# Optimization experiments

Hardware: AMD Instinct MI355X
Metric: run time of the kernel (lower is better)

The kernel has to match this reference:

```python
import jax, jax.numpy as jnp
import numpy as np

D = 768
CTX = 64


def ln(x, g, b, eps=1e-5):
    m = x.mean(-1, keepdims=True)
    v = jnp.mean((x - m) ** 2, -1, keepdims=True)
    return (x - m) / jnp.sqrt(v + eps) * g + b


def setup_inputs() -> dict:
    key = jax.random.key(0)
    ks = jax.random.split(key, 16)
    B, N = 16, 1024
    w = lambda k, shape: jax.random.normal(k, shape, dtype=jnp.float32) * 0.02
    return {
        'comps': jax.random.normal(ks[0], (8, B, N, D), jnp.float32),
        'geometric_context': jax.random.normal(ks[1], (B, N, D), jnp.float32),
        'question_features': jax.random.normal(ks[2], (B, D), jnp.float32),
        'spatial_mask': jax.random.randint(ks[3], (B,), 0, 2) > 0,
        'gp_w1': w(ks[4], (D, D // 2)), 'gp_b1': jnp.zeros((D // 2,)),
        'gp_g1': jnp.ones((D // 2,)), 'gp_be1': jnp.zeros((D // 2,)),
        'gp_w2': w(ks[5], (D // 2, CTX)), 'gp_b2': jnp.zeros((CTX,)),
        'swp_w1': w(ks[6], (CTX + D, 256)), 'swp_b1': jnp.zeros((256,)),
        'swp_g1': jnp.ones((256,)), 'swp_be1': jnp.zeros((256,)),
        'swp_w2': w(ks[7], (256, 128)), 'swp_b2': jnp.zeros((128,)),
        'swp_g2': jnp.ones((128,)), 'swp_be2': jnp.zeros((128,)),
        'swp_w3': w(ks[8], (128, 8)), 'swp_b3': jnp.zeros((8,)),
        'sw1': w(ks[9], (4, D + CTX, D)), 'sb1': jnp.zeros((4, D)),
        'sg1': jnp.ones((4, D)), 'sbe1': jnp.zeros((4, D)),
        'sw2': w(ks[10], (4, D, D)), 'sb2': jnp.zeros((4, D)),
        'sg2': jnp.ones((4, D)), 'sbe2': jnp.zeros((4, D)),
        'rw1': w(ks[11], (4, D + CTX, D)), 'rb1': jnp.zeros((4, D)),
        'rg1': jnp.ones((4, D)), 'rbe1': jnp.zeros((4, D)),
        'rw2': w(ks[12], (4, D, D)), 'rb2': jnp.zeros((4, D)),
    }


def reference(comps, geometric_context, question_features, spatial_mask,
              gp_w1, gp_b1, gp_g1, gp_be1, gp_w2, gp_b2,
              swp_w1, swp_b1, swp_g1, swp_be1, swp_w2, swp_b2, swp_g2, swp_be2, swp_w3, swp_b3,
              sw1, sb1, sg1, sbe1, sw2, sb2, sg2, sbe2,
              rw1, rb1, rg1, rbe1, rw2, rb2):
    B, N = geometric_context.shape[:2]
    # geometric_processor on mean-pooled context -> [B, 64]
    gcc = jax.nn.relu(ln(geometric_context.mean(1) @ gp_w1 + gp_b1, gp_g1, gp_be1)) @ gp_w2 + gp_b2
    # spatial_weight_predictor -> softmax weights [B, 8]
    wi = jnp.concatenate([gcc, question_features], -1)
    h = jax.nn.gelu(ln(wi @ swp_w1 + swp_b1, swp_g1, swp_be1), approximate=False)
    h = jax.nn.gelu(ln(h @ swp_w2 + swp_b2, swp_g2, swp_be2), approximate=False)
    aw = jax.nn.softmax(h @ swp_w3 + swp_b3, -1)
    # expanded context; non-spatial samples use 0.1-scaled context for spatial-set comps
    ctx = jnp.broadcast_to(gcc[:, None, :], (B, N, CTX))
    ctx_s = ctx * jnp.where(spatial_mask, 1.0, 0.1)[:, None, None]
    # strong enhancers (GELU, second LN): P_unique(0), V_unique(1), PV(3), PT(5) - all spatial-set
    xs = jnp.concatenate([comps[jnp.array([0, 1, 3, 5])],
                          jnp.broadcast_to(ctx_s, (4, B, N, CTX))], -1)
    h = jax.nn.gelu(ln(jnp.einsum('kbnd,kdf->kbnf', xs, sw1) + sb1[:, None, None, :],
                       sg1[:, None, None, :], sbe1[:, None, None, :]), approximate=False)
    ys = ln(jnp.einsum('kbnd,kdf->kbnf', h, sw2) + sb2[:, None, None, :],
            sg2[:, None, None, :], sbe2[:, None, None, :])
    # ReLU enhancers (moderate/minimal share structure): TV(4, scaled ctx), T_unique(2), redundant(6), higher(7)
    ctx_r = jnp.stack([ctx_s, ctx, ctx, ctx], 0)
    xr = jnp.concatenate([comps[jnp.array([4, 2, 6, 7])], ctx_r], -1)
    h = jax.nn.relu(ln(jnp.einsum('kbnd,kdf->kbnf', xr, rw1) + rb1[:, None, None, :],
                       rg1[:, None, None, :], rbe1[:, None, None, :]))
    yr = jnp.einsum('kbnd,kdf->kbnf', h, rw2) + rb2[:, None, None, :]
    # non-spatial components pass through when spatial_mask is False
    m = spatial_mask[:, None, None]
    out = jnp.stack([
        ys[0],                              # P_unique
        ys[1],                              # V_unique
        jnp.where(m, yr[1], comps[2]),      # T_unique
        ys[2],                              # PV_synergy
        yr[0],                              # TV_synergy
        ys[3],                              # PT_synergy
        jnp.where(m, yr[2], comps[6]),      # redundant
        jnp.where(m, yr[3], comps[7]),      # higher_synergy
    ], 0)
    return out, aw
```

## Files before the change

### kernel.cpp

```cpp
#include <hip/hip_runtime.h>
#include <math.h>

#define MT 16384
#define DD 768
#define AW_OFF ((size_t)8 * MT * DD)

typedef __attribute__((ext_vector_type(8))) short short8;
typedef __attribute__((ext_vector_type(4))) float f32x4;
typedef __attribute__((ext_vector_type(4))) float fv4;
typedef __attribute__((ext_vector_type(4))) unsigned int u32x4;

#define OFF_W1T 0ULL
#define OFF_W2T 9437184ULL
#define OFF_Z1  19660800ULL
#define OFF_Z2  220987392ULL
#define OFF_P1  321650688ULL
#define OFF_P2  327942144ULL
#define OFF_ST1 331087872ULL
#define OFF_ST2 332136448ULL
#define OFF_GP  332660736ULL
#define OFF_GM  333053952ULL
#define OFF_CXF 333103104ULL
#define OFF_B1X 333111296ULL
#define OFF_A1  335544320ULL
#define OFF_CB  536870912ULL

static __device__ __forceinline__ unsigned short f2bf(float f) {
  unsigned u = __float_as_uint(f);
  u += 0x7fffu + ((u >> 16) & 1u);
  return (unsigned short)(u >> 16);
}
static __device__ __forceinline__ float bf2f(unsigned short h) {
  return __uint_as_float(((unsigned)h) << 16);
}
static __device__ __forceinline__ unsigned pk2(float lo, float hi) {
  return (unsigned)f2bf(lo) | ((unsigned)f2bf(hi) << 16);
}
static __device__ __forceinline__ float gelu_t(float y) {
  float y2 = y * y;
  float c = fmaf(y2, 0.0713548163f, 1.59576912161f);
  float e = __expf(-y * c);
  return y / (1.0f + e);
}
static __device__ __forceinline__ void gload_lds16(const void* g, void* l) {
  __builtin_amdgcn_global_load_lds(
      (const __attribute__((address_space(1))) void*)g,
      (__attribute__((address_space(3))) void*)l, 16, 0, 0);
}

__global__ void cvt_comps(const float* __restrict__ c,
                          unsigned short* __restrict__ cb, long n8) {
  long i = (long)blockIdx.x * blockDim.x + threadIdx.x;
  const long stride = (long)gridDim.x * blockDim.x;
  for (; i < n8; i += stride) {
    const fv4* p = (const fv4*)(c + i * 8);
    fv4 a = p[0], b = p[1];
    u32x4 v;
    v[0] = pk2(a[0], a[1]); v[1] = pk2(a[2], a[3]);
    v[2] = pk2(b[0], b[1]); v[3] = pk2(b[2], b[3]);
    *(u32x4*)(cb + i * 8) = v;
  }
}

__global__ void transpose_cvt(const float* sw1, const float* rw1,
                              const float* sw2, const float* rw2,
                              unsigned short* w1T, unsigned short* w2T) {
  __shared__ float t[32][33];
  const int z = blockIdx.z;
  const float* sp; unsigned short* dp;
  if (z < 8) {
    sp = ((z < 4) ? sw1 : rw1) + (size_t)(z & 3) * 832 * DD;
    dp = w1T + (size_t)z * DD * DD;
  } else {
    int zz = z - 8;
    sp = ((zz < 4) ? sw2 : rw2) + (size_t)(zz & 3) * DD * DD;
    dp = w2T + (size_t)zz * DD * DD;
  }
  const int r0 = blockIdx.x * 32, c0 = blockIdx.y * 32;
  const int tx = threadIdx.x & 31, ty = threadIdx.x >> 5;
#pragma unroll
  for (int i = 0; i < 4; i++) {
    int r = ty + i * 8;
    t[r][tx] = sp[(size_t)(r0 + r) * DD + c0 + tx];
  }
  __syncthreads();
#pragma unroll
  for (int i = 0; i < 4; i++) {
    int cc = ty + i * 8;
    dp[(size_t)(c0 + cc) * DD + r0 + tx] = f2bf(t[tx][cc]);
  }
}

__global__ void colmean1(const float* __restrict__ geo, float* __restrict__ gp) {
  const int b = blockIdx.z, yc = blockIdx.y;
  const int col = blockIdx.x * 256 + threadIdx.x;
  const float* p = geo + (size_t)b * 1024 * DD + (size_t)yc * 128 * DD + col;
  float s = 0.f;
  for (int n = 0; n < 128; ++n) s += p[(size_t)n * DD];
  gp[((size_t)b * 8 + yc) * DD + col] = s;
}
__global__ void colmean2(const float* __restrict__ gp, float* __restrict__ gm) {
  const int b = blockIdx.y;
  const int col = blockIdx.x * 256 + threadIdx.x;
  float s = 0.f;
#pragma unroll
  for (int i = 0; i < 8; ++i) s += gp[((size_t)b * 8 + i) * DD + col];
  gm[(size_t)b * DD + col] = s * (1.0f / 1024.0f);
}

static __device__ float2 blk_sum2(float a, float b, float* red) {
  const int tid = threadIdx.x;
  __syncthreads();
  red[tid] = a; red[512 + tid] = b;
  if (tid < 128) { red[384 + tid] = 0.f; red[512 + 384 + tid] = 0.f; }
  __syncthreads();
  for (int s = 256; s > 0; s >>= 1) {
    if (tid < s) { red[tid] += red[tid + s]; red[512 + tid] += red[512 + tid + s]; }
    __syncthreads();
  }
  return make_float2(red[0], red[512]);
}

__global__ void small_mlp(
    const float* __restrict__ gc_mean, const float* __restrict__ qf,
    const int* __restrict__ mask,
    const float* __restrict__ gp_w1, const float* __restrict__ gp_b1,
    const float* __restrict__ gp_g1, const float* __restrict__ gp_be1,
    const float* __restrict__ gp_w2, const float* __restrict__ gp_b2,
    const float* __restrict__ swp_w1, const float* __restrict__ swp_b1,
    const float* __restrict__ swp_g1, const float* __restrict__ swp_be1,
    const float* __restrict__ swp_w2, const float* __restrict__ swp_b2,
    const float* __restrict__ swp_g2, const float* __restrict__ swp_be2,
    const float* __restrict__ swp_w3, const float* __restrict__ swp_b3,
    float* __restrict__ cxfs, float* __restrict__ cxfu,
    float* __restrict__ aw)
{
  __shared__ float gm[768];
  __shared__ float buf[832];
  __shared__ float tmp[384];
  __shared__ float red[1024];
  const int b = blockIdx.x, tid = threadIdx.x;

  for (int i = tid; i < 768; i += 384) gm[i] = gc_mean[b * 768 + i];
  __syncthreads();

  float z = gp_b1[tid];
  for (int k = 0; k < 768; k++) z += gm[k] * gp_w1[k * 384 + tid];
  float2 s = blk_sum2(z, z * z, red);
  {
    float mean = s.x * (1.f / 384.f);
    float rinv = rsqrtf(s.y * (1.f / 384.f) - mean * mean + 1e-5f);
    float y = (z - mean) * rinv * gp_g1[tid] + gp_be1[tid];
    tmp[tid] = fmaxf(y, 0.f);
  }
  __syncthreads();

  if (tid < 64) {
    float g = gp_b2[tid];
    for (int k = 0; k < 384; k++) g += tmp[k] * gp_w2[k * 64 + tid];
    float sc = (mask[b] != 0) ? 1.0f : 0.1f;
    cxfs[b * 64 + tid] = g * sc;
    cxfu[b * 64 + tid] = g;
    buf[tid] = g;
  }
  for (int i = tid; i < 768; i += 384) buf[64 + i] = qf[b * 768 + i];
  __syncthreads();

  float z1 = 0.f;
  if (tid < 256) {
    z1 = swp_b1[tid];
    for (int k = 0; k < 832; k++) z1 += buf[k] * swp_w1[k * 256 + tid];
  }
  s = blk_sum2(z1, z1 * z1, red);
  {
    float mean = s.x * (1.f / 256.f);
    float rinv = rsqrtf(s.y * (1.f / 256.f) - mean * mean + 1e-5f);
    if (tid < 256) {
      float y = (z1 - mean) * rinv * swp_g1[tid] + swp_be1[tid];
      tmp[tid] = 0.5f * y * (1.f + erff(y * 0.7071067811865476f));
    }
  }
  __syncthreads();

  float z2 = 0.f;
  if (tid < 128) {
    z2 = swp_b2[tid];
    for (int k = 0; k < 256; k++) z2 += tmp[k] * swp_w2[k * 128 + tid];
  }
  s = blk_sum2(z2, z2 * z2, red);
  {
    float mean = s.x * (1.f / 128.f);
    float rinv = rsqrtf(s.y * (1.f / 128.f) - mean * mean + 1e-5f);
    if (tid < 128) {
      float y = (z2 - mean) * rinv * swp_g2[tid] + swp_be2[tid];
      tmp[tid] = 0.5f * y * (1.f + erff(y * 0.7071067811865476f));
    }
  }
  __syncthreads();

  if (tid < 8) {
    float z3 = swp_b3[tid];
    for (int k = 0; k < 128; k++) z3 += tmp[k] * swp_w3[k * 8 + tid];
    buf[tid] = z3;
  }
  __syncthreads();
  if (tid < 8) {
    float mx = buf[0];
    for (int k = 1; k < 8; k++) mx = fmaxf(mx, buf[k]);
    float ssum = 0.f;
    for (int k = 0; k < 8; k++) ssum += expf(buf[k] - mx);
    aw[b * 8 + tid] = expf(buf[tid] - mx) / ssum;
  }
}

__global__ void ctxbias_k(const float* __restrict__ cxfs,
                          const float* __restrict__ cxfu,
                          const float* __restrict__ sw1, const float* __restrict__ rw1,
                          const float* __restrict__ sb1, const float* __restrict__ rb1,
                          float* __restrict__ b1x)
{
  const int br = blockIdx.x, b = blockIdx.y, tid = threadIdx.x;
  __shared__ float cf[64];
  if (tid < 64) cf[tid] = ((br <= 4) ? cxfs : cxfu)[b * 64 + tid];
  __syncthreads();
  const float* W = ((br < 4) ? sw1 + (size_t)br * 832 * DD
                             : rw1 + (size_t)(br - 4) * 832 * DD) + (size_t)768 * DD;
  const float* bb = (br < 4) ? sb1 + br * DD : rb1 + (br - 4) * DD;
#pragma unroll
  for (int jj = 0; jj < 3; ++jj) {
    const int f = tid + jj * 256;
    float s = bb[f];
    for (int k = 0; k < 64; ++k) s += cf[k] * W[(size_t)k * DD + f];
    b1x[((size_t)br * 16 + b) * DD + f] = s;
  }
}

__global__ void stats_k(const float2* __restrict__ part, float2* __restrict__ st,
                        int nr) {
  int i = blockIdx.x * 256 + threadIdx.x;
  if (i >= nr) return;
  float s1 = 0.f, s2 = 0.f;
#pragma unroll
  for (int s = 0; s < 3; ++s) {
    float2 p = part[(size_t)s * nr + i];
    s1 += p.x; s2 += p.y;
  }
  float mean = s1 * (1.f / 768.f);
  float var = s2 * (1.f / 768.f) - mean * mean;
  float rinv = rsqrtf(var + 1e-5f);
  st[i] = make_float2(rinv, -mean * rinv);
}

__global__ __launch_bounds__(512, 4)
void gemm1_k(const unsigned short* __restrict__ compsb,
             const unsigned short* __restrict__ w1T,
             const float* __restrict__ b1x,
             unsigned short* __restrict__ z1,
             float2* __restrict__ part1,
             const int* __restrict__ mask)
{
  __shared__ __align__(16) unsigned short As[3][4096];
  __shared__ __align__(16) unsigned short Bs[3][8192];
  __shared__ float pscr[4][128][2];
  constexpr int NT = 24;

  const int id = blockIdx.x;
  const int x = id & 7, j = id >> 3;
  const int br_nt = j >> 4;
  const int mt = ((j & 15) << 3) | x;
  const int nt = br_nt % 3;
  const int br = br_nt / 3;
  const int m0 = mt * 128, n0 = nt * 256;
  const int b = m0 >> 10;
  if (br >= 5 && mask[b] == 0) return;

  const int ci = (0x76245310u >> (br * 4)) & 15;
  const unsigned short* az = compsb + (size_t)ci * MT * DD + (size_t)m0 * DD;
  const unsigned short* wT = w1T + (size_t)br * DD * DD + (size_t)n0 * DD;

  const int tid = threadIdx.x;
  const int w = tid >> 6, lane = tid & 63, llo = lane & 15, lhi = lane >> 4;
  const int wm = w & 1, wn = w >> 1;
  const int q = lane & 3, rrB = w * 16 + (lane >> 2);
  const int swqB = q ^ ((rrB >> 1) & 3);

  const unsigned short* asrcD = az + (size_t)rrB * DD + swqB * 8;
  const unsigned short* bsrc0 = wT + (size_t)rrB * DD + swqB * 8;
  const unsigned short* bsrc1 = wT + (size_t)(128 + rrB) * DD + swqB * 8;

  f32x4 acc[4][4];
#pragma unroll
  for (int mf = 0; mf < 4; ++mf)
#pragma unroll
    for (int nf = 0; nf < 4; ++nf) acc[mf][nf] = (f32x4)0.0f;

  auto issueT = [&](int kt, int s) {
    gload_lds16(asrcD + (size_t)kt * 32, &As[s][w * 512]);
    gload_lds16(bsrc0 + (size_t)kt * 32, &Bs[s][w * 512]);
    gload_lds16(bsrc1 + (size_t)kt * 32, &Bs[s][4096 + w * 512]);
  };

  const int aswz = (lhi ^ ((llo >> 1) & 3)) << 3;
  const int arow0 = (wm * 64 + llo) * 32 + aswz;
  const int brow0 = (wn * 64 + llo) * 32 + aswz;
  auto compute = [&](int sl) {
    short8 afr[4];
#pragma unroll
    for (int mf = 0; mf < 4; ++mf)
      afr[mf] = *(const short8*)&As[sl][arow0 + mf * 512];
#pragma unroll
    for (int nf = 0; nf < 4; ++nf) {
      short8 bfr = *(const short8*)&Bs[sl][brow0 + nf * 512];
#pragma unroll
      for (int mf = 0; mf < 4; ++mf)
        acc[mf][nf] = __builtin_amdgcn_mfma_f32_16x16x32_bf16(afr[mf], bfr, acc[mf][nf], 0, 0, 0);
    }
  };

  issueT(0, 0);
  issueT(1, 1);
  asm volatile("s_waitcnt vmcnt(3)" ::: "memory");
  __builtin_amdgcn_sched_barrier(0);
  __builtin_amdgcn_s_barrier();

  int sc = 0;
#pragma unroll 1
  for (int t = 0; t < NT; ++t) {
    int s2 = sc + 2; if (s2 >= 3) s2 -= 3;
    const bool more = (t + 2 < NT);
    if (more) issueT(t + 2, s2);
    __builtin_amdgcn_sched_barrier(0);
    compute(sc);
    if (more) asm volatile("s_waitcnt vmcnt(3)" ::: "memory");
    else      asm volatile("s_waitcnt vmcnt(0)" ::: "memory");
    asm volatile("s_waitcnt lgkmcnt(0)" ::: "memory");
    __builtin_amdgcn_sched_barrier(0);
    __builtin_amdgcn_s_barrier();
    ++sc; if (sc == 3) sc = 0;
  }

  const float* bias = b1x + ((size_t)br * 16 + b) * DD;
  unsigned short* zo = z1 + (size_t)br * MT * DD + (size_t)m0 * DD;
  const int n0w = n0 + wn * 64;
  float bia[4];
#pragma unroll
  for (int nf = 0; nf < 4; ++nf) bia[nf] = bias[n0w + nf * 16 + llo];
#pragma unroll
  for (int mf = 0; mf < 4; ++mf) {
#pragma unroll
    for (int r = 0; r < 4; ++r) {
      float zz[4]; float s1v = 0.f, s2v = 0.f;
#pragma unroll
      for (int nf = 0; nf < 4; ++nf) {
        float zv = acc[mf][nf][r] + bia[nf];
        zz[nf] = zv; s1v += zv; s2v += zv * zv;
      }
      const int rloc = wm * 64 + mf * 16 + lhi * 4 + r;
      const size_t rowoff = (size_t)rloc * DD;
#pragma unroll
      for (int nf = 0; nf < 4; ++nf) {
        float zon = __shfl_xor(zz[nf], 1);
        if ((llo & 1) == 0)
          *(unsigned*)&zo[rowoff + n0w + nf * 16 + llo] = pk2(zz[nf], zon);
      }
#pragma unroll
      for (int d = 1; d < 16; d <<= 1) {
        s1v += __shfl_xor(s1v, d); s2v += __shfl_xor(s2v, d);
      }
      if (llo == 0) { pscr[wn][rloc][0] = s1v; pscr[wn][rloc][1] = s2v; }
    }
  }
  __syncthreads();
  if (tid < 128) {
    float a = 0.f, c = 0.f;
#pragma unroll
    for (int qq = 0; qq < 4; ++qq) { a += pscr[qq][tid][0]; c += pscr[qq][tid][1]; }
    part1[(size_t)nt * (8 * MT) + (size_t)br * MT + m0 + tid] = make_float2(a, c);
  }
}

__global__ void act1_k(const unsigned short* __restrict__ z1,
                       const float2* __restrict__ st1,
                       const float* __restrict__ sg1, const float* __restrict__ sbe1,
                       const float* __restrict__ rg1, const float* __restrict__ rbe1,
                       const int* __restrict__ mask,
                       unsigned short* __restrict__ a1)
{
  const int tid = threadIdx.x;
  const int rowg = blockIdx.x * 8 + (tid >> 5);
  const int l = tid & 31;
  const int br = rowg >> 14;
  const int r = rowg & 16383;
  const int b = r >> 10;
  if (br >= 5 && mask[b] == 0) return;
  const bool isg = (br < 4);
  const float* g  = (isg ? sg1  + br * DD : rg1  + (br - 4) * DD);
  const float* be = (isg ? sbe1 + br * DD : rbe1 + (br - 4) * DD);
  const float2 stv = st1[rowg];
  const unsigned short* zp = z1 + (size_t)rowg * DD;
  unsigned short* op = a1 + (size_t)rowg * DD;
#pragma unroll
  for (int c = 0; c < 3; ++c) {
    const int col = l * 8 + c * 256;
    u32x4 zv = *(const u32x4*)(zp + col);
    fv4 ga = *(const fv4*)(g + col), gb = *(const fv4*)(g + col + 4);
    fv4 ba = *(const fv4*)(be + col), bb = *(const fv4*)(be + col + 4);
    float y[8];
#pragma unroll
    for (int wd = 0; wd < 2; ++wd) {
      y[2*wd]   = fmaf(fmaf(bf2f((unsigned short)(zv[wd] & 0xffffu)), stv.x, stv.y), ga[2*wd], ba[2*wd]);
      y[2*wd+1] = fmaf(fmaf(bf2f((unsigned short)(zv[wd] >> 16)), stv.x, stv.y), ga[2*wd+1], ba[2*wd+1]);
      y[4+2*wd]   = fmaf(fmaf(bf2f((unsigned short)(zv[wd+2] & 0xffffu)), stv.x, stv.y), gb[2*wd], bb[2*wd]);
      y[4+2*wd+1] = fmaf(fmaf(bf2f((unsigned short)(zv[wd+2] >> 16)), stv.x, stv.y), gb[2*wd+1], bb[2*wd+1]);
    }
    u32x4 ov;
#pragma unroll
    for (int wd = 0; wd < 4; ++wd) {
      float y0 = y[2*wd], y1 = y[2*wd+1];
      if (isg) { y0 = gelu_t(y0); y1 = gelu_t(y1); }
      else     { y0 = fmaxf(y0, 0.f); y1 = fmaxf(y1, 0.f); }
      ov[wd] = pk2(y0, y1);
    }
    *(u32x4*)(op + col) = ov;
  }
}

__global__ __launch_bounds__(512, 4)
void gemm2_k(const float* __restrict__ comps,
             const unsigned short* __restrict__ a1,
             const unsigned short* __restrict__ w2T,
             const float* __restrict__ sb2, const float* __restrict__ rb2,
             unsigned short* __restrict__ z2,
             float2* __restrict__ part2,
             float* __restrict__ outp,
             const int* __restrict__ mask)
{
  __shared__ __align__(16) unsigned short As[3][4096];
  __shared__ __align__(16) unsigned short Bs[3][8192];
  __shared__ float pscr[4][128][2];
  constexpr int NT = 24;

  const int id = blockIdx.x;
  const int x = id & 7, j = id >> 3;
  const int br_nt = j >> 4;
  const int mt = ((j & 15) << 3) | x;
  const int nt = br_nt % 3;
  const int br = br_nt / 3;
  const int m0 = mt * 128, n0 = nt * 256;
  const int b = m0 >> 10;
  const int ci = (0x76245310u >> (br * 4)) & 15;
  const int tid = threadIdx.x;

  if (br >= 5 && mask[b] == 0) {
    const float* cs = comps + (size_t)ci * MT * DD + (size_t)m0 * DD + n0;
    float* cd = outp + (size_t)ci * MT * DD + (size_t)m0 * DD + n0;
#pragma unroll 1
    for (int k = 0; k < 16; ++k) {
      int idx = tid + k * 512;
      int r2 = idx >> 6, c4 = (idx & 63) * 4;
      *(fv4*)(cd + (size_t)r2 * DD + c4) = *(const fv4*)(cs + (size_t)r2 * DD + c4);
    }
    return;
  }

  const unsigned short* az = a1 + (size_t)br * MT * DD + (size_t)m0 * DD;
  const unsigned short* wT = w2T + (size_t)br * DD * DD + (size_t)n0 * DD;

  const int w = tid >> 6, lane = tid & 63, llo = lane & 15, lhi = lane >> 4;
  const int wm = w & 1, wn = w >> 1;
  const int q = lane & 3, rrB = w * 16 + (lane >> 2);
  const int swqB = q ^ ((rrB >> 1) & 3);

  const unsigned short* asrcD = az + (size_t)rrB * DD + swqB * 8;
  const unsigned short* bsrc0 = wT + (size_t)rrB * DD + swqB * 8;
  const unsigned short* bsrc1 = wT + (size_t)(128 + rrB) * DD + swqB * 8;

  f32x4 acc[4][4];
#pragma unroll
  for (int mf = 0; mf < 4; ++mf)
#pragma unroll
    for (int nf = 0; nf < 4; ++nf) acc[mf][nf] = (f32x4)0.0f;

  auto issueT = [&](int kt, int s) {
    gload_lds16(asrcD + (size_t)kt * 32, &As[s][w * 512]);
    gload_lds16(bsrc0 + (size_t)kt * 32, &Bs[s][w * 512]);
    gload_lds16(bsrc1 + (size_t)kt * 32, &Bs[s][4096 + w * 512]);
  };

  const int aswz = (lhi ^ ((llo >> 1) & 3)) << 3;
  const int arow0 = (wm * 64 + llo) * 32 + aswz;
  const int brow0 = (wn * 64 + llo) * 32 + aswz;
  auto compute = [&](int sl) {
    short8 afr[4];
#pragma unroll
    for (int mf = 0; mf < 4; ++mf)
      afr[mf] = *(const short8*)&As[sl][arow0 + mf * 512];
#pragma unroll
    for (int nf = 0; nf < 4; ++nf) {
      short8 bfr = *(const short8*)&Bs[sl][brow0 + nf * 512];
#pragma unroll
      for (int mf = 0; mf < 4; ++mf)
        acc[mf][nf] = __builtin_amdgcn_mfma_f32_16x16x32_bf16(afr[mf], bfr, acc[mf][nf], 0, 0, 0);
    }
  };

  issueT(0, 0);
  issueT(1, 1);
  asm volatile("s_waitcnt vmcnt(3)" ::: "memory");
  __builtin_amdgcn_sched_barrier(0);
  __builtin_amdgcn_s_barrier();

  int sc = 0;
#pragma unroll 1
  for (int t = 0; t < NT; ++t) {
    int s2 = sc + 2; if (s2 >= 3) s2 -= 3;
    const bool more = (t + 2 < NT);
    if (more) issueT(t + 2, s2);
    __builtin_amdgcn_sched_barrier(0);
    compute(sc);
    if (more) asm volatile("s_waitcnt vmcnt(3)" ::: "memory");
    else      asm volatile("s_waitcnt vmcnt(0)" ::: "memory");
    asm volatile("s_waitcnt lgkmcnt(0)" ::: "memory");
    __builtin_amdgcn_sched_barrier(0);
    __builtin_amdgcn_s_barrier();
    ++sc; if (sc == 3) sc = 0;
  }

  const int n0w = n0 + wn * 64;
  const float* bias = ((br < 4) ? sb2 : rb2) + (br & 3) * DD;
  float bia[4];
#pragma unroll
  for (int nf = 0; nf < 4; ++nf) bia[nf] = bias[n0w + nf * 16 + llo];

  if (br < 4) {
    unsigned short* zo = z2 + (size_t)br * MT * DD + (size_t)m0 * DD;
#pragma unroll
    for (int mf = 0; mf < 4; ++mf) {
#pragma unroll
      for (int r = 0; r < 4; ++r) {
        float zz[4]; float s1v = 0.f, s2v = 0.f;
#pragma unroll
        for (int nf = 0; nf < 4; ++nf) {
          float zv = acc[mf][nf][r] + bia[nf];
          zz[nf] = zv; s1v += zv; s2v += zv * zv;
        }
        const int rloc = wm * 64 + mf * 16 + lhi * 4 + r;
        const size_t rowoff = (size_t)rloc * DD;
#pragma unroll
        for (int nf = 0; nf < 4; ++nf) {
          float zon = __shfl_xor(zz[nf], 1);
          if ((llo & 1) == 0)
            *(unsigned*)&zo[rowoff + n0w + nf * 16 + llo] = pk2(zz[nf], zon);
        }
#pragma unroll
        for (int d = 1; d < 16; d <<= 1) {
          s1v += __shfl_xor(s1v, d); s2v += __shfl_xor(s2v, d);
        }
        if (llo == 0) { pscr[wn][rloc][0] = s1v; pscr[wn][rloc][1] = s2v; }
      }
    }
    __syncthreads();
    if (tid < 128) {
      float a = 0.f, c = 0.f;
#pragma unroll
      for (int qq = 0; qq < 4; ++qq) { a += pscr[qq][tid][0]; c += pscr[qq][tid][1]; }
      part2[(size_t)nt * (4 * MT) + (size_t)br * MT + m0 + tid] = make_float2(a, c);
    }
  } else {
    float* fo = outp + (size_t)ci * MT * DD + (size_t)m0 * DD;
#pragma unroll
    for (int mf = 0; mf < 4; ++mf) {
#pragma unroll
      for (int r = 0; r < 4; ++r) {
        const int rloc = wm * 64 + mf * 16 + lhi * 4 + r;
        const size_t rowoff = (size_t)rloc * DD;
#pragma unroll
        for (int nf = 0; nf < 4; ++nf)
          fo[rowoff + n0w + nf * 16 + llo] = acc[mf][nf][r] + bia[nf];
      }
    }
  }
}

__global__ void finish_s(const unsigned short* __restrict__ z2,
                         const float2* __restrict__ st2,
                         const float* __restrict__ sg2,
                         const float* __restrict__ sbe2,
                         float* __restrict__ outp)
{
  const int tid = threadIdx.x;
  const int rowg = blockIdx.x * 8 + (tid >> 5);
  const int l = tid & 31;
  const int br = rowg >> 14;
  const int r = rowg & 16383;
  const int ci = (0x5310u >> (br * 4)) & 15;
  const unsigned short* zp = z2 + (size_t)rowg * DD;
  float* op = outp + (size_t)ci * MT * DD + (size_t)r * DD;
  const float2 stv = st2[rowg];
  const float* g = sg2 + br * DD;
  const float* be = sbe2 + br * DD;
#pragma unroll
  for (int c = 0; c < 3; ++c) {
    const int col = l * 8 + c * 256;
    u32x4 zv = *(const u32x4*)(zp + col);
    fv4 ga = *(const fv4*)(g + col), gb = *(const fv4*)(g + col + 4);
    fv4 ba = *(const fv4*)(be + col), bb = *(const fv4*)(be + col + 4);
    fv4 o0, o1;
#pragma unroll
    for (int wd = 0; wd < 2; ++wd) {
      o0[2 * wd]     = fmaf(fmaf(bf2f((unsigned short)(zv[wd] & 0xffffu)), stv.x, stv.y), ga[2 * wd], ba[2 * wd]);
      o0[2 * wd + 1] = fmaf(fmaf(bf2f((unsigned short)(zv[wd] >> 16)), stv.x, stv.y), ga[2 * wd + 1], ba[2 * wd + 1]);
      o1[2 * wd]     = fmaf(fmaf(bf2f((unsigned short)(zv[wd + 2] & 0xffffu)), stv.x, stv.y), gb[2 * wd], bb[2 * wd]);
      o1[2 * wd + 1] = fmaf(fmaf(bf2f((unsigned short)(zv[wd + 2] >> 16)), stv.x, stv.y), gb[2 * wd + 1], bb[2 * wd + 1]);
    }
    *(fv4*)(op + col) = o0;
    *(fv4*)(op + col + 4) = o1;
  }
}

extern "C" void kernel_launch(void* const* d_in, const int* in_sizes, int n_in,
                              void* d_out, int out_size, void* d_ws, size_t ws_size,
                              hipStream_t stream)
{
  (void)in_sizes; (void)n_in; (void)out_size; (void)ws_size;
  const float* comps  = (const float*)d_in[0];
  const float* geo    = (const float*)d_in[1];
  const float* qf     = (const float*)d_in[2];
  const int*   mask   = (const int*)d_in[3];
  const float* gp_w1  = (const float*)d_in[4];
  const float* gp_b1  = (const float*)d_in[5];
  const float* gp_g1  = (const float*)d_in[6];
  const float* gp_be1 = (const float*)d_in[7];
  const float* gp_w2  = (const float*)d_in[8];
  const float* gp_b2  = (const float*)d_in[9];
  const float* swp_w1 = (const float*)d_in[10];
  const float* swp_b1 = (const float*)d_in[11];
  const float* swp_g1 = (const float*)d_in[12];
  const float* swp_be1= (const float*)d_in[13];
  const float* swp_w2 = (const float*)d_in[14];
  const float* swp_b2 = (const float*)d_in[15];
  const float* swp_g2 = (const float*)d_in[16];
  const float* swp_be2= (const float*)d_in[17];
  const float* swp_w3 = (const float*)d_in[18];
  const float* swp_b3 = (const float*)d_in[19];
  const float* sw1 = (const float*)d_in[20];
  const float* sb1 = (const float*)d_in[21];
  const float* sg1 = (const float*)d_in[22];
  const float* sbe1= (const float*)d_in[23];
  const float* sw2 = (const float*)d_in[24];
  const float* sb2 = (const float*)d_in[25];
  const float* sg2 = (const float*)d_in[26];
  const float* sbe2= (const float*)d_in[27];
  const float* rw1 = (const float*)d_in[28];
  const float* rb1 = (const float*)d_in[29];
  const float* rg1 = (const float*)d_in[30];
  const float* rbe1= (const float*)d_in[31];
  const float* rw2 = (const float*)d_in[32];
  const float* rb2 = (const float*)d_in[33];
  float* out = (float*)d_out;

  char* ws = (char*)d_ws;
  unsigned short* w1T = (unsigned short*)(ws + OFF_W1T);
  unsigned short* w2T = (unsigned short*)(ws + OFF_W2T);
  unsigned short* z1  = (unsigned short*)(ws + OFF_Z1);
  unsigned short* z2  = (unsigned short*)(ws + OFF_Z2);
  float2* part1 = (float2*)(ws + OFF_P1);
  float2* part2 = (float2*)(ws + OFF_P2);
  float2* st1   = (float2*)(ws + OFF_ST1);
  float2* st2   = (float2*)(ws + OFF_ST2);
  float* gpart  = (float*)(ws + OFF_GP);
  float* gmean  = (float*)(ws + OFF_GM);
  float* cxfs   = (float*)(ws + OFF_CXF);
  float* cxfu   = (float*)(ws + OFF_CXF + 4096);
  float* b1x    = (float*)(ws + OFF_B1X);
  unsigned short* a1     = (unsigned short*)(ws + OFF_A1);
  unsigned short* compsb = (unsigned short*)(ws + OFF_CB);

  cvt_comps<<<2048, 256, 0, stream>>>(comps, compsb, (long)8 * MT * DD / 8);
  transpose_cvt<<<dim3(24, 24, 16), 256, 0, stream>>>(sw1, rw1, sw2, rw2, w1T, w2T);
  colmean1<<<dim3(3, 8, 16), 256, 0, stream>>>(geo, gpart);
  colmean2<<<dim3(3, 16), 256, 0, stream>>>(gpart, gmean);
  small_mlp<<<16, 384, 0, stream>>>(gmean, qf, mask,
      gp_w1, gp_b1, gp_g1, gp_be1, gp_w2, gp_b2,
      swp_w1, swp_b1, swp_g1, swp_be1, swp_w2, swp_b2, swp_g2, swp_be2,
      swp_w3, swp_b3, cxfs, cxfu, out + AW_OFF);
  ctxbias_k<<<dim3(8, 16), 256, 0, stream>>>(cxfs, cxfu, sw1, rw1, sb1, rb1, b1x);

  gemm1_k<<<3072, 512, 0, stream>>>(compsb, w1T, b1x, z1, part1, mask);
  stats_k<<<512, 256, 0, stream>>>(part1, st1, 8 * MT);
  act1_k<<<16384, 256, 0, stream>>>(z1, st1, sg1, sbe1, rg1, rbe1, mask, a1);
  gemm2_k<<<3072, 512, 0, stream>>>(comps, a1, w2T, sb2, rb2, z2, part2, out, mask);
  stats_k<<<256, 256, 0, stream>>>(part2, st2, 4 * MT);
  finish_s<<<8192, 256, 0, stream>>>(z2, st2, sg2, sbe2, out);
}
```

Baseline: 855.3 us.

## Enlarge GEMM tiles to 256x256 with K=64 double-buffered pipeline

Both branch GEMMs now use 256x256 output tiles with a 64-wide K step, double-buffered LDS staging, an XOR swizzle, and 8x4 MFMA accumulators per wave, replacing the 128x256, K=32 triple-buffered scheme. Larger tiles raise arithmetic intensity and halve global reloads of A/B per output. The inner loop adds barriers and s_setprio around MFMA bursts to interleave waves. The cost is more registers and LDS per block (occupancy drops to 2 blocks), half as many blocks, and more barrier synchronisation.

```diff
diff --git a/kernel.cpp b/kernel.cpp
--- a/kernel.cpp
+++ b/kernel.cpp
@@ -251,7 +251,76 @@
   st[i] = make_float2(rinv, -mean * rinv);
 }
 
-__global__ __launch_bounds__(512, 4)
+#define GEMM_CORE(AZ, BZ)                                                     \
+  const int tid = threadIdx.x;                                                \
+  const int w = tid >> 6, lane = tid & 63, llo = lane & 15, lhi = lane >> 4;  \
+  const int wm = w >> 2, wn = w & 3;                                          \
+  const unsigned short* asrc[4]; const unsigned short* bsrc[4];               \
+  int dstc[4];                                                                \
+  _Pragma("unroll")                                                           \
+  for (int j = 0; j < 4; ++j) {                                               \
+    int cl = j * 512 + tid; int row = cl >> 3, c = cl & 7;                    \
+    asrc[j] = (AZ) + (size_t)row * DD + ((c ^ (row & 7)) << 3);               \
+    bsrc[j] = (BZ) + (size_t)row * DD + ((c ^ (row & 7)) << 3);               \
+    dstc[j] = (j * 512 + w * 64) * 8;                                         \
+  }                                                                           \
+  f32x4 acc[8][4];                                                            \
+  _Pragma("unroll")                                                           \
+  for (int mf = 0; mf < 8; ++mf)                                              \
+    _Pragma("unroll")                                                         \
+    for (int nf = 0; nf < 4; ++nf) acc[mf][nf] = (f32x4)0.0f;                 \
+  const int a0 = wm * 8192 + llo * 64;                                        \
+  const int b0 = wn * 4096 + llo * 64;                                        \
+  const int sw0 = (lhi ^ (llo & 7)) << 3;                                     \
+  const int sw1x = ((4 + lhi) ^ (llo & 7)) << 3;                              \
+  auto stage = [&](int kt, int nb) {                                          \
+    _Pragma("unroll")                                                         \
+    for (int j = 0; j < 4; ++j)                                               \
+      gload_lds16(asrc[j] + (size_t)kt * 64, &Abuf[nb][dstc[j]]);             \
+    _Pragma("unroll")                                                         \
+    for (int j = 0; j < 4; ++j)                                               \
+      gload_lds16(bsrc[j] + (size_t)kt * 64, &Bbuf[nb][dstc[j]]);             \
+  };                                                                          \
+  stage(0, 0);                                                                \
+  asm volatile("s_waitcnt vmcnt(0)" ::: "memory");                            \
+  __builtin_amdgcn_s_barrier();                                               \
+  _Pragma("unroll 1")                                                         \
+  for (int t = 0; t < 12; ++t) {                                              \
+    const int buf = t & 1;                                                    \
+    const unsigned short* Ab = &Abuf[buf][0];                                 \
+    const unsigned short* Bb = &Bbuf[buf][0];                                 \
+    if (t + 1 < 12) stage(t + 1, buf ^ 1);                                    \
+    short8 aF[8]; short8 bF0, bF1;                                            \
+    _Pragma("unroll")                                                         \
+    for (int ks = 0; ks < 2; ++ks) {                                          \
+      const int sw = ks ? sw1x : sw0;                                         \
+      _Pragma("unroll")                                                       \
+      for (int nh = 0; nh < 2; ++nh) {                                        \
+        if (nh == 0) {                                                        \
+          _Pragma("unroll")                                                   \
+          for (int mf = 0; mf < 8; ++mf)                                      \
+            aF[mf] = *(const short8*)&Ab[a0 + mf * 1024 + sw];                \
+        }                                                                     \
+        bF0 = *(const short8*)&Bb[b0 + (nh * 2 + 0) * 1024 + sw];             \
+        bF1 = *(const short8*)&Bb[b0 + (nh * 2 + 1) * 1024 + sw];             \
+        __builtin_amdgcn_s_barrier();                                         \
+        __builtin_amdgcn_s_setprio(1);                                        \
+        _Pragma("unroll")                                                     \
+        for (int mf = 0; mf < 8; ++mf) {                                      \
+          acc[mf][nh * 2 + 0] = __builtin_amdgcn_mfma_f32_16x16x32_bf16(      \
+              aF[mf], bF0, acc[mf][nh * 2 + 0], 0, 0, 0);                     \
+          acc[mf][nh * 2 + 1] = __builtin_amdgcn_mfma_f32_16x16x32_bf16(      \
+              aF[mf], bF1, acc[mf][nh * 2 + 1], 0, 0, 0);                     \
+        }                                                                     \
+        __builtin_amdgcn_s_setprio(0);                                        \
+        if (ks == 1 && nh == 1 && t + 1 < 12)                                 \
+          asm volatile("s_waitcnt vmcnt(0)" ::: "memory");                    \
+        __builtin_amdgcn_s_barrier();                                         \
+      }                                                                       \
+    }                                                                         \
+  }
+
+__global__ __launch_bounds__(512, 2)
 void gemm1_k(const unsigned short* __restrict__ compsb,
              const unsigned short* __restrict__ w1T,
              const float* __restrict__ b1x,
@@ -259,94 +328,33 @@
              float2* __restrict__ part1,
              const int* __restrict__ mask)
 {
-  __shared__ __align__(16) unsigned short As[3][4096];
-  __shared__ __align__(16) unsigned short Bs[3][8192];
-  __shared__ float pscr[4][128][2];
-  constexpr int NT = 24;
+  __shared__ __align__(16) unsigned short Abuf[2][16384];
+  __shared__ __align__(16) unsigned short Bbuf[2][16384];
+  __shared__ float pscr[4][256][2];
 
   const int id = blockIdx.x;
   const int x = id & 7, j = id >> 3;
-  const int br_nt = j >> 4;
-  const int mt = ((j & 15) << 3) | x;
+  const int br_nt = j >> 3;
+  const int mt = ((j & 7) << 3) | x;
   const int nt = br_nt % 3;
   const int br = br_nt / 3;
-  const int m0 = mt * 128, n0 = nt * 256;
+  const int m0 = mt * 256, n0 = nt * 256;
   const int b = m0 >> 10;
   if (br >= 5 && mask[b] == 0) return;
 
   const int ci = (0x76245310u >> (br * 4)) & 15;
-  const unsigned short* az = compsb + (size_t)ci * MT * DD + (size_t)m0 * DD;
-  const unsigned short* wT = w1T + (size_t)br * DD * DD + (size_t)n0 * DD;
-
-  const int tid = threadIdx.x;
-  const int w = tid >> 6, lane = tid & 63, llo = lane & 15, lhi = lane >> 4;
-  const int wm = w & 1, wn = w >> 1;
-  const int q = lane & 3, rrB = w * 16 + (lane >> 2);
-  const int swqB = q ^ ((rrB >> 1) & 3);
-
-  const unsigned short* asrcD = az + (size_t)rrB * DD + swqB * 8;
-  const unsigned short* bsrc0 = wT + (size_t)rrB * DD + swqB * 8;
-  const unsigned short* bsrc1 = wT + (size_t)(128 + rrB) * DD + swqB * 8;
-
-  f32x4 acc[4][4];
-#pragma unroll
-  for (int mf = 0; mf < 4; ++mf)
-#pragma unroll
-    for (int nf = 0; nf < 4; ++nf) acc[mf][nf] = (f32x4)0.0f;
-
-  auto issueT = [&](int kt, int s) {
-    gload_lds16(asrcD + (size_t)kt * 32, &As[s][w * 512]);
-    gload_lds16(bsrc0 + (size_t)kt * 32, &Bs[s][w * 512]);
-    gload_lds16(bsrc1 + (size_t)kt * 32, &Bs[s][4096 + w * 512]);
-  };
-
-  const int aswz = (lhi ^ ((llo >> 1) & 3)) << 3;
-  const int arow0 = (wm * 64 + llo) * 32 + aswz;
-  const int brow0 = (wn * 64 + llo) * 32 + aswz;
-  auto compute = [&](int sl) {
-    short8 afr[4];
-#pragma unroll
-    for (int mf = 0; mf < 4; ++mf)
-      afr[mf] = *(const short8*)&As[sl][arow0 + mf * 512];
-#pragma unroll
-    for (int nf = 0; nf < 4; ++nf) {
-      short8 bfr = *(const short8*)&Bs[sl][brow0 + nf * 512];
-#pragma unroll
-      for (int mf = 0; mf < 4; ++mf)
-        acc[mf][nf] = __builtin_amdgcn_mfma_f32_16x16x32_bf16(afr[mf], bfr, acc[mf][nf], 0, 0, 0);
-    }
-  };
-
-  issueT(0, 0);
-  issueT(1, 1);
-  asm volatile("s_waitcnt vmcnt(3)" ::: "memory");
-  __builtin_amdgcn_sched_barrier(0);
-  __builtin_amdgcn_s_barrier();
-
-  int sc = 0;
-#pragma unroll 1
-  for (int t = 0; t < NT; ++t) {
-    int s2 = sc + 2; if (s2 >= 3) s2 -= 3;
-    const bool more = (t + 2 < NT);
-    if (more) issueT(t + 2, s2);
-    __builtin_amdgcn_sched_barrier(0);
-    compute(sc);
-    if (more) asm volatile("s_waitcnt vmcnt(3)" ::: "memory");
-    else      asm volatile("s_waitcnt vmcnt(0)" ::: "memory");
-    asm volatile("s_waitcnt lgkmcnt(0)" ::: "memory");
-    __builtin_amdgcn_sched_barrier(0);
-    __builtin_amdgcn_s_barrier();
-    ++sc; if (sc == 3) sc = 0;
-  }
+  const unsigned short* aG = compsb + (size_t)ci * MT * DD + (size_t)m0 * DD;
+  const unsigned short* bG = w1T + (size_t)br * DD * DD + (size_t)n0 * DD;
+
+  GEMM_CORE(aG, bG)
 
   const float* bias = b1x + ((size_t)br * 16 + b) * DD;
   unsigned short* zo = z1 + (size_t)br * MT * DD + (size_t)m0 * DD;
-  const int n0w = n0 + wn * 64;
   float bia[4];
 #pragma unroll
-  for (int nf = 0; nf < 4; ++nf) bia[nf] = bias[n0w + nf * 16 + llo];
-#pragma unroll
-  for (int mf = 0; mf < 4; ++mf) {
+  for (int nf = 0; nf < 4; ++nf) bia[nf] = bias[n0 + wn * 64 + nf * 16 + llo];
+#pragma unroll
+  for (int mf = 0; mf < 8; ++mf) {
 #pragma unroll
     for (int r = 0; r < 4; ++r) {
       float zz[4]; float s1v = 0.f, s2v = 0.f;
@@ -355,13 +363,13 @@
         float zv = acc[mf][nf][r] + bia[nf];
         zz[nf] = zv; s1v += zv; s2v += zv * zv;
       }
-      const int rloc = wm * 64 + mf * 16 + lhi * 4 + r;
+      const int rloc = wm * 128 + mf * 16 + lhi * 4 + r;
       const size_t rowoff = (size_t)rloc * DD;
 #pragma unroll
       for (int nf = 0; nf < 4; ++nf) {
         float zon = __shfl_xor(zz[nf], 1);
         if ((llo & 1) == 0)
-          *(unsigned*)&zo[rowoff + n0w + nf * 16 + llo] = pk2(zz[nf], zon);
+          *(unsigned*)&zo[rowoff + n0 + wn * 64 + nf * 16 + llo] = pk2(zz[nf], zon);
       }
 #pragma unroll
       for (int d = 1; d < 16; d <<= 1) {
@@ -371,7 +379,7 @@
     }
   }
   __syncthreads();
-  if (tid < 128) {
+  if (tid < 256) {
     float a = 0.f, c = 0.f;
 #pragma unroll
     for (int qq = 0; qq < 4; ++qq) { a += pscr[qq][tid][0]; c += pscr[qq][tid][1]; }
@@ -425,7 +433,7 @@
   }
 }
 
-__global__ __launch_bounds__(512, 4)
+__global__ __launch_bounds__(512, 2)
 void gemm2_k(const float* __restrict__ comps,
              const unsigned short* __restrict__ a1,
              const unsigned short* __restrict__ w2T,
@@ -435,107 +443,47 @@
              float* __restrict__ outp,
              const int* __restrict__ mask)
 {
-  __shared__ __align__(16) unsigned short As[3][4096];
-  __shared__ __align__(16) unsigned short Bs[3][8192];
-  __shared__ float pscr[4][128][2];
-  constexpr int NT = 24;
+  __shared__ __align__(16) unsigned short Abuf[2][16384];
+  __shared__ __align__(16) unsigned short Bbuf[2][16384];
+  __shared__ float pscr[4][256][2];
 
   const int id = blockIdx.x;
   const int x = id & 7, j = id >> 3;
-  const int br_nt = j >> 4;
-  const int mt = ((j & 15) << 3) | x;
+  const int br_nt = j >> 3;
+  const int mt = ((j & 7) << 3) | x;
   const int nt = br_nt % 3;
   const int br = br_nt / 3;
-  const int m0 = mt * 128, n0 = nt * 256;
+  const int m0 = mt * 256, n0 = nt * 256;
   const int b = m0 >> 10;
   const int ci = (0x76245310u >> (br * 4)) & 15;
-  const int tid = threadIdx.x;
 
   if (br >= 5 && mask[b] == 0) {
+    const int tid0 = threadIdx.x;
     const float* cs = comps + (size_t)ci * MT * DD + (size_t)m0 * DD + n0;
     float* cd = outp + (size_t)ci * MT * DD + (size_t)m0 * DD + n0;
 #pragma unroll 1
-    for (int k = 0; k < 16; ++k) {
-      int idx = tid + k * 512;
+    for (int k = 0; k < 32; ++k) {
+      int idx = tid0 + k * 512;
       int r2 = idx >> 6, c4 = (idx & 63) * 4;
       *(fv4*)(cd + (size_t)r2 * DD + c4) = *(const fv4*)(cs + (size_t)r2 * DD + c4);
     }
     return;
   }
 
-  const unsigned short* az = a1 + (size_t)br * MT * DD + (size_t)m0 * DD;
-  const unsigned short* wT = w2T + (size_t)br * DD * DD + (size_t)n0 * DD;
-
-  const int w = tid >> 6, lane = tid & 63, llo = lane & 15, lhi = lane >> 4;
-  const int wm = w & 1, wn = w >> 1;
-  const int q = lane & 3, rrB = w * 16 + (lane >> 2);
-  const int swqB = q ^ ((rrB >> 1) & 3);
-
-  const unsigned short* asrcD = az + (size_t)rrB * DD + swqB * 8;
-  const unsigned short* bsrc0 = wT + (size_t)rrB * DD + swqB * 8;
-  const unsigned short* bsrc1 = wT + (size_t)(128 + rrB) * DD + swqB * 8;
-
-  f32x4 acc[4][4];
-#pragma unroll
-  for (int mf = 0; mf < 4; ++mf)
-#pragma unroll
-    for (int nf = 0; nf < 4; ++nf) acc[mf][nf] = (f32x4)0.0f;
-
-  auto issueT = [&](int kt, int s) {
-    gload_lds16(asrcD + (size_t)kt * 32, &As[s][w * 512]);
-    gload_lds16(bsrc0 + (size_t)kt * 32, &Bs[s][w * 512]);
-    gload_lds16(bsrc1 + (size_t)kt * 32, &Bs[s][4096 + w * 512]);
-  };
-
-  const int aswz = (lhi ^ ((llo >> 1) & 3)) << 3;
-  const int arow0 = (wm * 64 + llo) * 32 + aswz;
-  const int brow0 = (wn * 64 + llo) * 32 + aswz;
-  auto compute = [&](int sl) {
-    short8 afr[4];
-#pragma unroll
-    for (int mf = 0; mf < 4; ++mf)
-      afr[mf] = *(const short8*)&As[sl][arow0 + mf * 512];
-#pragma unroll
-    for (int nf = 0; nf < 4; ++nf) {
-      short8 bfr = *(const short8*)&Bs[sl][brow0 + nf * 512];
-#pragma unroll
-      for (int mf = 0; mf < 4; ++mf)
-        acc[mf][nf] = __builtin_amdgcn_mfma_f32_16x16x32_bf16(afr[mf], bfr, acc[mf][nf], 0, 0, 0);
-    }
-  };
-
-  issueT(0, 0);
-  issueT(1, 1);
-  asm volatile("s_waitcnt vmcnt(3)" ::: "memory");
-  __builtin_amdgcn_sched_barrier(0);
-  __builtin_amdgcn_s_barrier();
-
-  int sc = 0;
-#pragma unroll 1
-  for (int t = 0; t < NT; ++t) {
-    int s2 = sc + 2; if (s2 >= 3) s2 -= 3;
-    const bool more = (t + 2 < NT);
-    if (more) issueT(t + 2, s2);
-    __builtin_amdgcn_sched_barrier(0);
-    compute(sc);
-    if (more) asm volatile("s_waitcnt vmcnt(3)" ::: "memory");
-    else      asm volatile("s_waitcnt vmcnt(0)" ::: "memory");
-    asm volatile("s_waitcnt lgkmcnt(0)" ::: "memory");
-    __builtin_amdgcn_sched_barrier(0);
-    __builtin_amdgcn_s_barrier();
-    ++sc; if (sc == 3) sc = 0;
-  }
-
-  const int n0w = n0 + wn * 64;
+  const unsigned short* aG = a1 + (size_t)br * MT * DD + (size_t)m0 * DD;
+  const unsigned short* bG = w2T + (size_t)br * DD * DD + (size_t)n0 * DD;
+
+  GEMM_CORE(aG, bG)
+
   const float* bias = ((br < 4) ? sb2 : rb2) + (br & 3) * DD;
   float bia[4];
 #pragma unroll
-  for (int nf = 0; nf < 4; ++nf) bia[nf] = bias[n0w + nf * 16 + llo];
+  for (int nf = 0; nf < 4; ++nf) bia[nf] = bias[n0 + wn * 64 + nf * 16 + llo];
 
   if (br < 4) {
     unsigned short* zo = z2 + (size_t)br * MT * DD + (size_t)m0 * DD;
 #pragma unroll
-    for (int mf = 0; mf < 4; ++mf) {
+    for (int mf = 0; mf < 8; ++mf) {
 #pragma unroll
       for (int r = 0; r < 4; ++r) {
         float zz[4]; float s1v = 0.f, s2v = 0.f;
@@ -544,13 +492,13 @@
           float zv = acc[mf][nf][r] + bia[nf];
           zz[nf] = zv; s1v += zv; s2v += zv * zv;
         }
-        const int rloc = wm * 64 + mf * 16 + lhi * 4 + r;
+        const int rloc = wm * 128 + mf * 16 + lhi * 4 + r;
         const size_t rowoff = (size_t)rloc * DD;
 #pragma unroll
         for (int nf = 0; nf < 4; ++nf) {
           float zon = __shfl_xor(zz[nf], 1);
           if ((llo & 1) == 0)
-            *(unsigned*)&zo[rowoff + n0w + nf * 16 + llo] = pk2(zz[nf], zon);
+            *(unsigned*)&zo[rowoff + n0 + wn * 64 + nf * 16 + llo] = pk2(zz[nf], zon);
         }
 #pragma unroll
         for (int d = 1; d < 16; d <<= 1) {
@@ -560,7 +508,7 @@
       }
     }
     __syncthreads();
-    if (tid < 128) {
+    if (tid < 256) {
       float a = 0.f, c = 0.f;
 #pragma unroll
       for (int qq = 0; qq < 4; ++qq) { a += pscr[qq][tid][0]; c += pscr[qq][tid][1]; }
@@ -569,14 +517,14 @@
   } else {
     float* fo = outp + (size_t)ci * MT * DD + (size_t)m0 * DD;
 #pragma unroll
-    for (int mf = 0; mf < 4; ++mf) {
+    for (int mf = 0; mf < 8; ++mf) {
 #pragma unroll
       for (int r = 0; r < 4; ++r) {
-        const int rloc = wm * 64 + mf * 16 + lhi * 4 + r;
+        const int rloc = wm * 128 + mf * 16 + lhi * 4 + r;
         const size_t rowoff = (size_t)rloc * DD;
 #pragma unroll
         for (int nf = 0; nf < 4; ++nf)
-          fo[rowoff + n0w + nf * 16 + llo] = acc[mf][nf][r] + bia[nf];
+          fo[rowoff + n0 + wn * 64 + nf * 16 + llo] = acc[mf][nf][r] + bia[nf];
       }
     }
   }
@@ -686,10 +634,10 @@
       swp_w3, swp_b3, cxfs, cxfu, out + AW_OFF);
   ctxbias_k<<<dim3(8, 16), 256, 0, stream>>>(cxfs, cxfu, sw1, rw1, sb1, rb1, b1x);
 
-  gemm1_k<<<3072, 512, 0, stream>>>(compsb, w1T, b1x, z1, part1, mask);
+  gemm1_k<<<1536, 512, 0, stream>>>(compsb, w1T, b1x, z1, part1, mask);
   stats_k<<<512, 256, 0, stream>>>(part1, st1, 8 * MT);
   act1_k<<<16384, 256, 0, stream>>>(z1, st1, sg1, sbe1, rg1, rbe1, mask, a1);
-  gemm2_k<<<3072, 512, 0, stream>>>(comps, a1, w2T, sb2, rb2, z2, part2, out, mask);
+  gemm2_k<<<1536, 512, 0, stream>>>(comps, a1, w2T, sb2, rb2, z2, part2, out, mask);
   stats_k<<<256, 256, 0, stream>>>(part2, st2, 4 * MT);
   finish_s<<<8192, 256, 0, stream>>>(z2, st2, sg2, sbe2, out);
 }
```

New measurement: 976.6 us. +14.2%, slower.

## Fuse fp32-to-bf16 conversion of comps into gemm1 A-tile loading

Applied to the files above, without the earlier changes.

Removes the standalone cvt_comps kernel and its bf16 workspace copy; gemm1 now loads fp32 A rows into registers, packs them to bf16 and stores them into swizzled LDS. The pipeline changes from three-stage async LDS loads to a two-stage scheme with register staging for A. This removes a full read/write pass over comps at the cost of doubled A bytes per GEMM tile load and less prefetch depth.

```diff
diff --git a/kernel.cpp b/kernel.cpp
--- a/kernel.cpp
+++ b/kernel.cpp
@@ -23,7 +23,6 @@
 #define OFF_CXF 333103104ULL
 #define OFF_B1X 333111296ULL
 #define OFF_A1  335544320ULL
-#define OFF_CB  536870912ULL
 
 static __device__ __forceinline__ unsigned short f2bf(float f) {
   unsigned u = __float_as_uint(f);
@@ -46,20 +45,6 @@
   __builtin_amdgcn_global_load_lds(
       (const __attribute__((address_space(1))) void*)g,
       (__attribute__((address_space(3))) void*)l, 16, 0, 0);
-}
-
-__global__ void cvt_comps(const float* __restrict__ c,
-                          unsigned short* __restrict__ cb, long n8) {
-  long i = (long)blockIdx.x * blockDim.x + threadIdx.x;
-  const long stride = (long)gridDim.x * blockDim.x;
-  for (; i < n8; i += stride) {
-    const fv4* p = (const fv4*)(c + i * 8);
-    fv4 a = p[0], b = p[1];
-    u32x4 v;
-    v[0] = pk2(a[0], a[1]); v[1] = pk2(a[2], a[3]);
-    v[2] = pk2(b[0], b[1]); v[3] = pk2(b[2], b[3]);
-    *(u32x4*)(cb + i * 8) = v;
-  }
 }
 
 __global__ void transpose_cvt(const float* sw1, const float* rw1,
@@ -252,15 +237,15 @@
 }
 
 __global__ __launch_bounds__(512, 4)
-void gemm1_k(const unsigned short* __restrict__ compsb,
+void gemm1_k(const float* __restrict__ comps,
              const unsigned short* __restrict__ w1T,
              const float* __restrict__ b1x,
              unsigned short* __restrict__ z1,
              float2* __restrict__ part1,
              const int* __restrict__ mask)
 {
-  __shared__ __align__(16) unsigned short As[3][4096];
-  __shared__ __align__(16) unsigned short Bs[3][8192];
+  __shared__ __align__(16) unsigned short As[2][4096];
+  __shared__ __align__(16) unsigned short Bs[2][8192];
   __shared__ float pscr[4][128][2];
   constexpr int NT = 24;
 
@@ -275,16 +260,19 @@
   if (br >= 5 && mask[b] == 0) return;
 
   const int ci = (0x76245310u >> (br * 4)) & 15;
-  const unsigned short* az = compsb + (size_t)ci * MT * DD + (size_t)m0 * DD;
+  const float* afp = comps + (size_t)ci * MT * DD + (size_t)m0 * DD;
   const unsigned short* wT = w1T + (size_t)br * DD * DD + (size_t)n0 * DD;
 
   const int tid = threadIdx.x;
   const int w = tid >> 6, lane = tid & 63, llo = lane & 15, lhi = lane >> 4;
   const int wm = w & 1, wn = w >> 1;
+
+  const int arow = tid >> 2, ap = tid & 3;
+  const int aslot = (arow * 32 + ((ap ^ ((arow >> 1) & 3)) << 3));
+  const float* asrc = afp + (size_t)arow * DD + ap * 8;
+
   const int q = lane & 3, rrB = w * 16 + (lane >> 2);
   const int swqB = q ^ ((rrB >> 1) & 3);
-
-  const unsigned short* asrcD = az + (size_t)rrB * DD + swqB * 8;
   const unsigned short* bsrc0 = wT + (size_t)rrB * DD + swqB * 8;
   const unsigned short* bsrc1 = wT + (size_t)(128 + rrB) * DD + swqB * 8;
 
@@ -294,10 +282,25 @@
 #pragma unroll
     for (int nf = 0; nf < 4; ++nf) acc[mf][nf] = (f32x4)0.0f;
 
-  auto issueT = [&](int kt, int s) {
-    gload_lds16(asrcD + (size_t)kt * 32, &As[s][w * 512]);
+  struct St { u32x4 q0, q1; };
+
+  auto issueB = [&](int kt, int s) {
     gload_lds16(bsrc0 + (size_t)kt * 32, &Bs[s][w * 512]);
     gload_lds16(bsrc1 + (size_t)kt * 32, &Bs[s][4096 + w * 512]);
+  };
+  auto loadA = [&](int kt) -> St {
+    St s;
+    const u32x4* p = (const u32x4*)(asrc + kt * 32);
+    s.q0 = p[0]; s.q1 = p[1];
+    return s;
+  };
+  auto commitA = [&](const St& s, int sl) {
+    u32x4 v;
+    v[0] = pk2(__uint_as_float(s.q0[0]), __uint_as_float(s.q0[1]));
+    v[1] = pk2(__uint_as_float(s.q0[2]), __uint_as_float(s.q0[3]));
+    v[2] = pk2(__uint_as_float(s.q1[0]), __uint_as_float(s.q1[1]));
+    v[3] = pk2(__uint_as_float(s.q1[2]), __uint_as_float(s.q1[3]));
+    *(u32x4*)&As[sl][aslot] = v;
   };
 
   const int aswz = (lhi ^ ((llo >> 1) & 3)) << 3;
@@ -317,26 +320,31 @@
     }
   };
 
-  issueT(0, 0);
-  issueT(1, 1);
-  asm volatile("s_waitcnt vmcnt(3)" ::: "memory");
+  issueB(0, 0);
+  {
+    St s0 = loadA(0);
+    commitA(s0, 0);
+  }
+  asm volatile("s_waitcnt lgkmcnt(0)" ::: "memory");
   __builtin_amdgcn_sched_barrier(0);
   __builtin_amdgcn_s_barrier();
 
-  int sc = 0;
 #pragma unroll 1
   for (int t = 0; t < NT; ++t) {
-    int s2 = sc + 2; if (s2 >= 3) s2 -= 3;
-    const bool more = (t + 2 < NT);
-    if (more) issueT(t + 2, s2);
+    const int cur = t & 1, nxt = cur ^ 1;
+    const bool more = (t + 1 < NT);
+    St sn;
+    if (more) {
+      issueB(t + 1, nxt);
+      sn = loadA(t + 1);
+    }
     __builtin_amdgcn_sched_barrier(0);
-    compute(sc);
-    if (more) asm volatile("s_waitcnt vmcnt(3)" ::: "memory");
-    else      asm volatile("s_waitcnt vmcnt(0)" ::: "memory");
+    compute(cur);
+    __builtin_amdgcn_sched_barrier(0);
+    if (more) commitA(sn, nxt);
     asm volatile("s_waitcnt lgkmcnt(0)" ::: "memory");
     __builtin_amdgcn_sched_barrier(0);
     __builtin_amdgcn_s_barrier();
-    ++sc; if (sc == 3) sc = 0;
   }
 
   const float* bias = b1x + ((size_t)br * 16 + b) * DD;
@@ -673,10 +681,8 @@
   float* cxfs   = (float*)(ws + OFF_CXF);
   float* cxfu   = (float*)(ws + OFF_CXF + 4096);
   float* b1x    = (float*)(ws + OFF_B1X);
-  unsigned short* a1     = (unsigned short*)(ws + OFF_A1);
-  unsigned short* compsb = (unsigned short*)(ws + OFF_CB);
-
-  cvt_comps<<<2048, 256, 0, stream>>>(comps, compsb, (long)8 * MT * DD / 8);
+  unsigned short* a1 = (unsigned short*)(ws + OFF_A1);
+
   transpose_cvt<<<dim3(24, 24, 16), 256, 0, stream>>>(sw1, rw1, sw2, rw2, w1T, w2T);
   colmean1<<<dim3(3, 8, 16), 256, 0, stream>>>(geo, gpart);
   colmean2<<<dim3(3, 16), 256, 0, stream>>>(gpart, gmean);
@@ -686,7 +692,7 @@
       swp_w3, swp_b3, cxfs, cxfu, out + AW_OFF);
   ctxbias_k<<<dim3(8, 16), 256, 0, stream>>>(cxfs, cxfu, sw1, rw1, sb1, rb1, b1x);
 
-  gemm1_k<<<3072, 512, 0, stream>>>(compsb, w1T, b1x, z1, part1, mask);
+  gemm1_k<<<3072, 512, 0, stream>>>(comps, w1T, b1x, z1, part1, mask);
   stats_k<<<512, 256, 0, stream>>>(part1, st1, 8 * MT);
   act1_k<<<16384, 256, 0, stream>>>(z1, st1, sg1, sbe1, rg1, rbe1, mask, a1);
   gemm2_k<<<3072, 512, 0, stream>>>(comps, a1, w2T, sb2, rb2, z2, part2, out, mask);
```

Measured after the change: 795.3 us. 7.0% less time.
